# Kernel tuning notes

Measured on AMD Instinct MI355X. Metric: run time of the kernel, lower is better.

## Reference

```python
import jax, jax.numpy as jnp
import numpy as np

H = 128   # d_model / features
N = 32    # kept complex modes (d_state=64 -> 32 conjugate pairs)
B = 8
L = 8192


def setup_inputs() -> dict:
    key = jax.random.key(0)
    ks = jax.random.split(key, 8)
    x = jax.random.normal(ks[0], (B, H, L), jnp.float32)
    # S4D (diagonal SSM) kernel parameters; channels=2 for bidirectional
    C_re = (jax.random.normal(ks[1], (2, H, N), jnp.float32) * (0.5 ** 0.5))
    C_im = (jax.random.normal(ks[2], (2, H, N), jnp.float32) * (0.5 ** 0.5))
    log_A_real = jnp.log(0.5 * jnp.ones((H, N), jnp.float32))          # S4D-Lin init
    A_imag = jnp.tile(np.pi * jnp.arange(N, dtype=jnp.float32), (H, 1))
    # log_dt uniform in [log(1e-3), log(1e-1)]
    u = jax.random.uniform(ks[3], (H,), jnp.float32)
    log_dt = u * (np.log(0.1) - np.log(0.001)) + np.log(0.001)
    D = jax.random.normal(ks[4], (H,), jnp.float32)                    # skip term
    W_pw = jax.random.normal(ks[5], (H, H), jnp.float32) / np.sqrt(H)  # 1x1 conv weight (out, in)
    gamma = jnp.ones((H,), jnp.float32)
    beta = jnp.zeros((H,), jnp.float32)
    return {"x": x, "C_re": C_re, "C_im": C_im, "log_A_real": log_A_real,
            "A_imag": A_imag, "log_dt": log_dt, "D": D, "W_pw": W_pw,
            "gamma": gamma, "beta": beta}


def reference(x, C_re, C_im, log_A_real, A_imag, log_dt, D, W_pw, gamma, beta):
    Lx = x.shape[-1]
    # ---- S4D SSM kernel via Vandermonde (ZOH discretization) ----
    A = -jnp.exp(log_A_real) + 1j * A_imag                 # (H, N) complex
    dt = jnp.exp(log_dt)[:, None]                          # (H, 1)
    dtA = A * dt                                           # (H, N)
    C = C_re + 1j * C_im                                   # (2, H, N)
    Kc = C * ((jnp.exp(dtA) - 1.0) / A)                    # (2, H, N)
    vand = jnp.exp(dtA[:, :, None] * jnp.arange(Lx))       # (H, N, L)
    k = 2.0 * jnp.einsum('chn,hnl->chl', Kc, vand).real    # (2, H, L)
    # ---- bidirectional: causal half + anticausal (flipped) half ----
    k_full = (jnp.pad(k[0], ((0, 0), (0, Lx)))
              + jnp.pad(k[1][:, ::-1], ((0, 0), (Lx, 0))))  # (H, 2L)
    # ---- FFT convolution ----
    n = 2 * Lx
    y = jnp.fft.irfft(jnp.fft.rfft(x, n=n) * jnp.fft.rfft(k_full, n=n), n=n)[..., :Lx]
    y = y + x * D[:, None]                                 # skip connection
    y = jax.nn.gelu(y, approximate=False)                  # FFTConv default activation
    # ---- pointwise 1x1 conv (no bias) ----
    y = jnp.einsum('bhl,oh->bol', y, W_pw)
    # ---- BatchNorm1d (training-mode batch statistics) ----
    mean = jnp.mean(y, axis=(0, 2), keepdims=True)
    var = jnp.var(y, axis=(0, 2), keepdims=True)
    y = (y - mean) * jax.lax.rsqrt(var + 1e-5) * gamma[:, None] + beta[:, None]
    # ---- ELU + residual (dropout p=0) ----
    return jax.nn.elu(y) + x
```

## Files before the change

kernel.cpp:

```cpp
#include <hip/hip_runtime.h>
#include <math.h>

#define HCH   128
#define NMODE 32
#define BB    8
#define LLEN  8192
#define LC    256
#define CCH   (LLEN / LC)
#define ROWS  (BB * HCH)

typedef unsigned int uint;
typedef _Float16 f16x8 __attribute__((ext_vector_type(8)));
typedef float    f32x4 __attribute__((ext_vector_type(4)));

static __device__ __forceinline__ uint pk2(float a, float b) {
    union { _Float16 h[2]; uint u; } v;
    v.h[0] = (_Float16)a; v.h[1] = (_Float16)b;
    return v.u;
}

__device__ __forceinline__ float gelu_f(float y) {
    float z = fabsf(y) * 0.7071067811865476f;
    float p = fmaf(z, 0.078108f, 0.000972f);
    p = fmaf(z, p, 0.230389f);
    p = fmaf(z, p, 0.278393f);
    p = fmaf(z, p, 1.0f);
    float p2 = p * p;
    float p4 = p2 * p2;
    float er = 1.f - __builtin_amdgcn_rcpf(p4);
    float s  = copysignf(er, y);
    return 0.5f * y * (1.f + s);
}

#define DPP_ADD(v, ctrl) { int _t = __builtin_amdgcn_update_dpp(0, __float_as_int(v), \
                             (ctrl), 0xF, 0xF, true); (v) += __int_as_float(_t); }

__global__ __launch_bounds__(256) void k_prep(const float* __restrict__ C_re,
                                              const float* __restrict__ C_im,
                                              const float* __restrict__ logA,
                                              const float* __restrict__ Aim,
                                              const float* __restrict__ logdt,
                                              const float* __restrict__ W,
                                              _Float16* __restrict__ aT,
                                              _Float16* __restrict__ eT,
                                              _Float16* __restrict__ Wh,
                                              float* __restrict__ Pw,
                                              float* __restrict__ stats) {
    __shared__ float2 PL[32 * 257];
    __shared__ float4 G01[32];
    __shared__ float4 HG[32];
    __shared__ float2 WL[32];
    __shared__ float k0L[256], k1L[256];
    int tid  = threadIdx.x;
    int h    = blockIdx.x >> 1;
    int half = blockIdx.x & 1;
    if (blockIdx.x == 0) stats[tid] = 0.f;
    if (half == 0 && tid < 128) Wh[h * 128 + tid] = (_Float16)W[h * 128 + tid];
    if (tid < 32) {
        int n = tid, idx = h * 32 + n;
        float ar = expf(logA[idx]);
        float ai = Aim[idx];
        float dt = expf(logdt[h]);
        float dre = -ar * dt, dim = ai * dt;
        float er = expf(dre);
        float wr = er * cosf(dim), wi = er * sinf(dim);
        WL[n] = (float2){wr, wi};
        if (half == 0) {
            float eL = expf(dre * 256.f);
            Pw[idx]        = eL * cosf(dim * 256.f);
            Pw[4096 + idx] = eL * sinf(dim * 256.f);
        }
        float den  = ar * ar + ai * ai;
        float numr = -(wr - 1.f) * ar + wi * ai;
        float numi = -wi * ar - (wr - 1.f) * ai;
        float Kr = numr / den, Ki = numi / den;
        float c0r = C_re[idx],        c0i = C_im[idx];
        float c1r = C_re[4096 + idx], c1i = C_im[4096 + idx];
        float g0r = 2.f * (c0r * Kr - c0i * Ki), g0i = 2.f * (c0r * Ki + c0i * Kr);
        float g1r = 2.f * (c1r * Kr - c1i * Ki);
        float g1i = 2.f * (c1r * Ki + c1i * Kr);
        G01[n] = (float4){g0r, g0i, g1r, g1i};
        HG[n]  = (float4){g0r * wr - g0i * wi, g0r * wi + g0i * wr, g1r, g1i};
    }
    __syncthreads();
    {
        int n = tid & 31, tg = tid >> 5;
        float2 w = WL[n];
        float w2r = w.x * w.x - w.y * w.y,   w2i = 2.f * w.x * w.y;
        float w4r = w2r * w2r - w2i * w2i,   w4i = 2.f * w2r * w2i;
        float w8r = w4r * w4r - w4i * w4i,   w8i = 2.f * w4r * w4i;
        float pr = (tg & 1) ? w.x : 1.f;
        float pi = (tg & 1) ? w.y : 0.f;
        if (tg & 2) { float t2 = pr * w2r - pi * w2i; pi = pr * w2i + pi * w2r; pr = t2; }
        if (tg & 4) { float t4 = pr * w4r - pi * w4i; pi = pr * w4i + pi * w4r; pr = t4; }
        float2* row = &PL[n * 257];
        #pragma unroll
        for (int j = 0; j < 32; j++) {
            row[tg + 8 * j] = (float2){pr, pi};
            float tr = pr * w8r - pi * w8i; pi = pr * w8i + pi * w8r; pr = tr;
        }
    }
    __syncthreads();
    {
        int tau = tid;
        float s0 = 0.f, s1 = 0.f;
        #pragma unroll
        for (int n = 0; n < 32; n++) {
            float2 p = PL[n * 257 + tau];
            float4 g = G01[n];
            s0 += g.x * p.x - g.y * p.y;
            s1 += g.z * p.x - g.w * p.y;
        }
        k0L[tau] = s0; k1L[tau] = s1;
    }
    __syncthreads();
    #pragma unroll 4
    for (int i = 0; i < 64; i++) {
        int idx = i * 256 + tid;
        int t  = half * 128 + (idx >> 7);
        int sp = (idx & 127) << 1;
        float v0 = (sp     <= t) ? k0L[t - sp]     : k1L[sp - t - 1];
        float v1 = (sp + 1 <= t) ? k0L[t - sp - 1] : k1L[sp - t];
        *(uint*)&aT[((size_t)(h * 256 + t)) * 384 + sp] = pk2(v0, v1);
    }
    #pragma unroll 4
    for (int i = 0; i < 16; i++) {
        int idx = i * 256 + tid;
        int n = idx & 31;
        int t = half * 128 + (idx >> 5);
        float2 pt = PL[n * 257 + t];
        float2 pu = PL[n * 257 + 255 - t];
        float4 hg = HG[n];
        size_t rb = ((size_t)(h * 256 + t)) * 384;
        *(uint*)&aT[rb + 256 + 2 * n] = pk2(hg.x * pt.x - hg.y * pt.y,
                                            -(hg.x * pt.y + hg.y * pt.x));
        *(uint*)&aT[rb + 320 + 2 * n] = pk2(hg.z * pu.x - hg.w * pu.y,
                                            -(hg.z * pu.y + hg.w * pu.x));
    }
    #pragma unroll 4
    for (int i = 0; i < 16; i++) {
        int idx = i * 256 + tid;
        int n = idx >> 7;
        int s = half * 128 + (idx & 127);
        float2 ps = PL[n * 257 + s];
        float2 pu = PL[n * 257 + 255 - s];
        size_t base = (size_t)h * 128 * 256;
        eT[base + (size_t)(2 * n) * 256 + s]      = (_Float16)pu.x;
        eT[base + (size_t)(2 * n + 1) * 256 + s]  = (_Float16)pu.y;
        eT[base + (size_t)(64 + 2 * n) * 256 + s] = (_Float16)ps.x;
        eT[base + (size_t)(65 + 2 * n) * 256 + s] = (_Float16)ps.y;
    }
}

__global__ __launch_bounds__(256, 2) void k_states_c(const float* __restrict__ x,
                                                     const _Float16* __restrict__ eT,
                                                     const float* __restrict__ Pw,
                                                     _Float16* __restrict__ xh,
                                                     _Float16* __restrict__ carr) {
    __shared__ _Float16 SM[4][5120];
    int tid = threadIdx.x;
    int xcd = blockIdx.x & 7, slot = blockIdx.x >> 3;
    int h = xcd * 16 + (slot >> 1), mt = slot & 1;
    int wave = tid >> 6, lane = tid & 63;
    int wm = wave >> 1, wn = wave & 1;
    int lrow = lane & 15, quad = lane >> 4;
    int koff = quad * 8;
    f32x4 acc[4][4];
    #pragma unroll
    for (int a = 0; a < 4; a++)
        #pragma unroll
        for (int b = 0; b < 4; b++) acc[a][b] = (f32x4){0.f, 0.f, 0.f, 0.f};

    const int chA = tid >> 3, segA = tid & 7;
    const size_t xbase = (((size_t)(mt * 4) * HCH + h) << 13) + (chA << 8) + segA * 4;
    const int rB = tid >> 2, sgB = tid & 3;

    float4 ar[4]; uint4 br[2];
    #define LOADA_S(kk) { _Pragma("unroll") for (int i = 0; i < 4; i++) \
        ar[i] = *(const float4*)(x + xbase + ((size_t)i << 20) + (kk)); }
    #define LOADB_S(kk) { _Pragma("unroll") for (int i = 0; i < 2; i++) \
        br[i] = *(const uint4*)(eT + ((size_t)(h * 128 + rB + 64 * i)) * 256 + (kk) + sgB * 8); }
    #define WRITE_S(buf, kk) { _Pragma("unroll") for (int i = 0; i < 4; i++) { \
            uint2 o; o.x = pk2(ar[i].x, ar[i].y); o.y = pk2(ar[i].z, ar[i].w); \
            *(uint2*)&SM[buf][(chA + 32 * i) * 40 + segA * 4] = o; \
            *(uint2*)&xh[xbase + ((size_t)i << 20) + (kk)] = o; } \
        _Pragma("unroll") for (int i = 0; i < 2; i++) \
            *(uint4*)&SM[2 + (buf)][(rB + 64 * i) * 40 + sgB * 8] = br[i]; }

    LOADA_S(0); LOADB_S(0);
    WRITE_S(0, 0);
    __syncthreads();
    for (int kt = 0; kt < 8; kt++) {
        int cur = kt & 1;
        if (kt < 7) { LOADA_S((kt + 1) * 32); LOADB_S((kt + 1) * 32); }
        f16x8 a[4], b[4];
        #pragma unroll
        for (int f = 0; f < 4; f++) {
            a[f] = *(const f16x8*)&SM[cur][(wm * 64 + f * 16 + lrow) * 40 + koff];
            b[f] = *(const f16x8*)&SM[2 + cur][(wn * 64 + f * 16 + lrow) * 40 + koff];
        }
        #pragma unroll
        for (int fi = 0; fi < 4; fi++)
            #pragma unroll
            for (int fj = 0; fj < 4; fj++)
                acc[fi][fj] = __builtin_amdgcn_mfma_f32_16x16x32_f16(a[fi], b[fj], acc[fi][fj], 0, 0, 0);
        if (kt < 7) {
            WRITE_S(cur ^ 1, (kt + 1) * 32);
            __syncthreads();
        }
    }
    __syncthreads();
    float* Sf = (float*)SM;
    #pragma unroll
    for (int p = 0; p < 2; p++) {
        if (wm == p) {
            #pragma unroll
            for (int fi = 0; fi < 4; fi++) {
                #pragma unroll
                for (int fj = 0; fj < 4; fj++) {
                    int srow = wn * 64 + fj * 16 + lrow;
                    #pragma unroll
                    for (int rg = 0; rg < 4; rg++) {
                        int lb = fi * 16 + quad * 4 + rg;
                        Sf[lb * 128 + srow] = acc[fi][fj][rg];
                    }
                }
            }
        }
        __syncthreads();
        if (tid < 128) {
            int blocL = tid >> 6, d = (tid >> 5) & 1, n = tid & 31;
            int bloc = p * 2 + blocL;
            float wLr = Pw[h * 32 + n], wLi = Pw[4096 + h * 32 + n];
            int srow = d * 64 + 2 * n;
            float cr = 0.f, ci = 0.f;
            size_t gb = ((size_t)(h * 256 + mt * 128 + bloc * 32)) * 128 + srow;
            if (d == 0) {
                for (int c = 0; c < CCH; c++) {
                    *(uint*)&carr[gb + (size_t)c * 128] = pk2(cr, ci);
                    float2 s = *(const float2*)&Sf[(blocL * 32 + c) * 128 + srow];
                    float nr = fmaf(wLr, cr, -wLi * ci) + s.x;
                    float ni = fmaf(wLi, cr,  wLr * ci) + s.y;
                    cr = nr; ci = ni;
                }
            } else {
                for (int c = CCH - 1; c >= 0; c--) {
                    *(uint*)&carr[gb + (size_t)c * 128] = pk2(cr, ci);
                    float2 s = *(const float2*)&Sf[(blocL * 32 + c) * 128 + srow];
                    float nr = fmaf(wLr, cr, -wLi * ci) + s.x;
                    float ni = fmaf(wLi, cr,  wLr * ci) + s.y;
                    cr = nr; ci = ni;
                }
            }
        }
        __syncthreads();
    }
    #undef LOADA_S
    #undef LOADB_S
    #undef WRITE_S
}

__global__ __launch_bounds__(256, 2) void k_conv_g(const _Float16* __restrict__ xh,
                                                   const _Float16* __restrict__ aT,
                                                   const _Float16* __restrict__ carr,
                                                   const float* __restrict__ D,
                                                   _Float16* __restrict__ Yg) {
    __shared__ _Float16 At[2][128 * 40];
    __shared__ _Float16 Bt[2][128 * 40];
    int tid = threadIdx.x;
    int xcd = blockIdx.x & 7, slot = blockIdx.x >> 3;
    int p = xcd * 32 + (slot >> 1);
    int mt = slot & 1;
    int h = p >> 1, nt = p & 1;
    int wave = tid >> 6, lane = tid & 63;
    int wm = wave >> 1, wn = wave & 1;
    int lrow = lane & 15, quad = lane >> 4;
    int koff = quad * 8;
    f32x4 acc[4][4];
    #pragma unroll
    for (int a = 0; a < 4; a++)
        #pragma unroll
        for (int b = 0; b < 4; b++) acc[a][b] = (f32x4){0.f, 0.f, 0.f, 0.f};

    const int rS = tid >> 2, sgS = tid & 3;

    uint4 a_r[2], b_r[2];
    #define LOADA_C(kk) { _Pragma("unroll") for (int i = 0; i < 2; i++) { \
            int bc = mt * 128 + rS + 64 * i; \
            a_r[i] = ((kk) < 256) \
              ? *(const uint4*)(xh + (((size_t)((bc >> 5) * HCH + h)) << 13) + ((bc & 31) << 8) + (kk) + sgS * 8) \
              : *(const uint4*)(carr + ((size_t)(h * 256 + bc)) * 128 + ((kk) - 256) + sgS * 8); } }
    #define LOADB_C(kk) { _Pragma("unroll") for (int i = 0; i < 2; i++) \
        b_r[i] = *(const uint4*)(aT + ((size_t)(h * 256 + nt * 128 + rS + 64 * i)) * 384 + (kk) + sgS * 8); }
    #define WRITE_C(buf) { _Pragma("unroll") for (int i = 0; i < 2; i++) { \
            *(uint4*)&At[buf][(rS + 64 * i) * 40 + sgS * 8] = a_r[i]; \
            *(uint4*)&Bt[buf][(rS + 64 * i) * 40 + sgS * 8] = b_r[i]; } }

    LOADA_C(0); LOADB_C(0);
    WRITE_C(0);
    __syncthreads();
    for (int kt = 0; kt < 12; kt++) {
        int cur = kt & 1;
        if (kt < 11) { LOADA_C((kt + 1) * 32); LOADB_C((kt + 1) * 32); }
        f16x8 a[4], b[4];
        #pragma unroll
        for (int f = 0; f < 4; f++) {
            a[f] = *(const f16x8*)&At[cur][(wm * 64 + f * 16 + lrow) * 40 + koff];
            b[f] = *(const f16x8*)&Bt[cur][(wn * 64 + f * 16 + lrow) * 40 + koff];
        }
        #pragma unroll
        for (int fi = 0; fi < 4; fi++)
            #pragma unroll
            for (int fj = 0; fj < 4; fj++)
                acc[fi][fj] = __builtin_amdgcn_mfma_f32_16x16x32_f16(a[fi], b[fj], acc[fi][fj], 0, 0, 0);
        if (kt < 11) {
            WRITE_C(cur ^ 1);
            __syncthreads();
        }
    }
    float Dh = D[h];
    #pragma unroll
    for (int fi = 0; fi < 4; fi++) {
        #pragma unroll
        for (int fj = 0; fj < 4; fj++) {
            int t = nt * 128 + wn * 64 + fj * 16 + lrow;
            #pragma unroll
            for (int rg = 0; rg < 4; rg++) {
                int bc = mt * 128 + wm * 64 + fi * 16 + quad * 4 + rg;
                size_t base = (((size_t)((bc >> 5) * HCH + h)) << 13) + ((bc & 31) << 8) + t;
                float xv = (float)xh[base];
                float yv = acc[fi][fj][rg] + Dh * xv;
                Yg[base] = (_Float16)gelu_f(yv);
            }
        }
    }
    #undef LOADA_C
    #undef LOADB_C
    #undef WRITE_C
}

__global__ __launch_bounds__(256, 2) void k_pointwise(const _Float16* __restrict__ Yg,
                                                      const _Float16* __restrict__ Wh,
                                                      _Float16* __restrict__ z,
                                                      float* __restrict__ stats) {
    __shared__ _Float16 Yt[2][128 * 40];
    __shared__ float Ls[512];
    int tid = threadIdx.x;
    int b  = blockIdx.x >> 6;
    int l0 = (blockIdx.x & 63) << 7;
    int wave = tid >> 6, lane = tid & 63;
    int wm = wave >> 1, wn = wave & 1;
    int lrow = lane & 15, quad = lane >> 4;
    int koff = quad * 8;
    f32x4 acc[4][4];
    #pragma unroll
    for (int a = 0; a < 4; a++)
        #pragma unroll
        for (int c = 0; c < 4; c++) acc[a][c] = (f32x4){0.f, 0.f, 0.f, 0.f};

    f16x8 a[4][4];
    #pragma unroll
    for (int ks = 0; ks < 4; ks++)
        #pragma unroll
        for (int f = 0; f < 4; f++)
            a[ks][f] = *(const f16x8*)(Wh + (wm * 64 + f * 16 + lrow) * HCH + ks * 32 + koff);

    const int hhS = tid & 31;
    const int lgbase = tid >> 5;
    uint4 yv[2];
    #define LOADY(kk) { _Pragma("unroll") for (int i = 0; i < 2; i++) \
        yv[i] = *(const uint4*)(Yg + (((size_t)(b * HCH + (kk) + hhS)) << 13) + l0 + (lgbase + 8 * i) * 8); }
    #define WRITEY(buf) { _Pragma("unroll") for (int i = 0; i < 2; i++) { \
            const _Float16* hv = (const _Float16*)&yv[i]; \
            _Pragma("unroll") for (int j = 0; j < 8; j++) \
                Yt[buf][((lgbase + 8 * i) * 8 + j) * 40 + hhS] = hv[j]; } }

    LOADY(0);
    WRITEY(0);
    __syncthreads();
    for (int kt = 0; kt < 4; kt++) {
        int cur = kt & 1;
        if (kt < 3) LOADY((kt + 1) * 32);
        f16x8 bf[4];
        #pragma unroll
        for (int f = 0; f < 4; f++)
            bf[f] = *(const f16x8*)&Yt[cur][(wn * 64 + f * 16 + lrow) * 40 + koff];
        #pragma unroll
        for (int fi = 0; fi < 4; fi++)
            #pragma unroll
            for (int fj = 0; fj < 4; fj++)
                acc[fi][fj] = __builtin_amdgcn_mfma_f32_16x16x32_f16(a[kt][fi], bf[fj], acc[fi][fj], 0, 0, 0);
        if (kt < 3) {
            WRITEY(cur ^ 1);
            __syncthreads();
        }
    }
    #pragma unroll
    for (int fi = 0; fi < 4; fi++) {
        #pragma unroll
        for (int fj = 0; fj < 4; fj++) {
            int l = l0 + wn * 64 + fj * 16 + lrow;
            #pragma unroll
            for (int rg = 0; rg < 4; rg++) {
                int o = wm * 64 + fi * 16 + quad * 4 + rg;
                z[(((size_t)(b * HCH + o)) << 13) + l] = (_Float16)acc[fi][fj][rg];
            }
        }
    }
    #pragma unroll
    for (int fi = 0; fi < 4; fi++) {
        #pragma unroll
        for (int rg = 0; rg < 4; rg++) {
            float s = 0.f, q = 0.f;
            #pragma unroll
            for (int fj = 0; fj < 4; fj++) {
                float v = acc[fi][fj][rg];
                s += v; q = fmaf(v, v, q);
            }
            DPP_ADD(s, 0xB1); DPP_ADD(s, 0x4E); DPP_ADD(s, 0x141); DPP_ADD(s, 0x140);
            DPP_ADD(q, 0xB1); DPP_ADD(q, 0x4E); DPP_ADD(q, 0x141); DPP_ADD(q, 0x140);
            if (lrow == 0) {
                int olo = fi * 16 + quad * 4 + rg;
                Ls[wave * 64 + olo]       = s;
                Ls[256 + wave * 64 + olo] = q;
            }
        }
    }
    __syncthreads();
    if (tid < HCH) {
        int wmn = tid >> 6;
        int olo = tid & 63;
        float s = Ls[(wmn * 2) * 64 + olo] + Ls[(wmn * 2 + 1) * 64 + olo];
        float q = Ls[256 + (wmn * 2) * 64 + olo] + Ls[256 + (wmn * 2 + 1) * 64 + olo];
        atomicAdd(&stats[tid], s);
        atomicAdd(&stats[HCH + tid], q);
    }
    #undef LOADY
    #undef WRITEY
}

__global__ __launch_bounds__(256) void k_final(const _Float16* __restrict__ z,
                                               const float* __restrict__ x,
                                               const float* __restrict__ stats,
                                               const float* __restrict__ gamma,
                                               const float* __restrict__ beta,
                                               float* __restrict__ out) {
    size_t i8 = (size_t)blockIdx.x * 256 + threadIdx.x;
    int o = (int)((i8 >> 10) & (HCH - 1));
    const float inv_cnt = 1.f / (float)(BB * LLEN);
    float m   = stats[o] * inv_cnt;
    float var = stats[HCH + o] * inv_cnt - m * m;
    float rs  = rsqrtf(var + 1e-5f);
    float ga  = gamma[o] * rs;
    float bt  = beta[o] - m * ga;
    uint4 zv = ((const uint4*)z)[i8];
    const _Float16* zh = (const _Float16*)&zv;
    float4 xa = ((const float4*)x)[2 * i8];
    float4 xb = ((const float4*)x)[2 * i8 + 1];
    float4 ra, rb;
    { float t = fmaf((float)zh[0], ga, bt); float e = t > 0.f ? t : (__expf(t) - 1.f); ra.x = e + xa.x; }
    { float t = fmaf((float)zh[1], ga, bt); float e = t > 0.f ? t : (__expf(t) - 1.f); ra.y = e + xa.y; }
    { float t = fmaf((float)zh[2], ga, bt); float e = t > 0.f ? t : (__expf(t) - 1.f); ra.z = e + xa.z; }
    { float t = fmaf((float)zh[3], ga, bt); float e = t > 0.f ? t : (__expf(t) - 1.f); ra.w = e + xa.w; }
    { float t = fmaf((float)zh[4], ga, bt); float e = t > 0.f ? t : (__expf(t) - 1.f); rb.x = e + xb.x; }
    { float t = fmaf((float)zh[5], ga, bt); float e = t > 0.f ? t : (__expf(t) - 1.f); rb.y = e + xb.y; }
    { float t = fmaf((float)zh[6], ga, bt); float e = t > 0.f ? t : (__expf(t) - 1.f); rb.z = e + xb.z; }
    { float t = fmaf((float)zh[7], ga, bt); float e = t > 0.f ? t : (__expf(t) - 1.f); rb.w = e + xb.w; }
    ((float4*)out)[2 * i8]     = ra;
    ((float4*)out)[2 * i8 + 1] = rb;
}

extern "C" void kernel_launch(void* const* d_in, const int* in_sizes, int n_in,
                              void* d_out, int out_size, void* d_ws, size_t ws_size,
                              hipStream_t stream) {
    const float* x     = (const float*)d_in[0];
    const float* C_re  = (const float*)d_in[1];
    const float* C_im  = (const float*)d_in[2];
    const float* logA  = (const float*)d_in[3];
    const float* Aim   = (const float*)d_in[4];
    const float* logdt = (const float*)d_in[5];
    const float* D     = (const float*)d_in[6];
    const float* W     = (const float*)d_in[7];
    const float* gamma = (const float*)d_in[8];
    const float* beta  = (const float*)d_in[9];

    float* ws = (float*)d_ws;
    _Float16* eT    = (_Float16*)ws;
    _Float16* Yg    = (_Float16*)ws;
    _Float16* aT    = (_Float16*)(ws + 8388608);
    _Float16* zf    = (_Float16*)(ws + 8388608);
    _Float16* carr  = (_Float16*)(ws + 16777216);
    float*    Pw    = ws + 16777216 + 2097152;
    float*    stats = Pw + 8192;
    _Float16* Wh    = (_Float16*)(ws + 18882880);
    _Float16* xh    = (_Float16*)(ws + 18891072);
    float*    out   = (float*)d_out;

    k_prep     <<<256,  256, 0, stream>>>(C_re, C_im, logA, Aim, logdt, W, aT, eT, Wh, Pw, stats);
    k_states_c <<<256,  256, 0, stream>>>(x, eT, Pw, xh, carr);
    k_conv_g   <<<512,  256, 0, stream>>>(xh, aT, carr, D, Yg);
    k_pointwise<<<512,  256, 0, stream>>>(Yg, Wh, zf, stats);
    k_final    <<<4096, 256, 0, stream>>>(zf, x, stats, gamma, beta, out);
}
```

Before: 175.5 us.

## Replace materialized Toeplitz kernel matrix with LDS-built Toeplitz fragments; split states kernel

The 256x256 Toeplitz block of the SSM kernel is no longer written to global memory per channel. Instead a compact 512-element packed kernel vector is stored, and the conv kernel builds the B fragments directly from LDS using shifted indices with even and odd packed copies. This removes large global write and read traffic for the Toeplitz operand. The states kernel is also split across two blocks per (h, mt), one per direction, doubling the grid and removing the serialized two-phase scan. The cost is extra LDS loads in the conv inner loop and duplicated x loads in the states kernel.

```diff
diff --git a/kernel.cpp b/kernel.cpp
--- a/kernel.cpp
+++ b/kernel.cpp
@@ -41,7 +41,8 @@
                                               const float* __restrict__ Aim,
                                               const float* __restrict__ logdt,
                                               const float* __restrict__ W,
-                                              _Float16* __restrict__ aT,
+                                              _Float16* __restrict__ cT,
+                                              uint* __restrict__ kmg,
                                               _Float16* __restrict__ eT,
                                               _Float16* __restrict__ Wh,
                                               float* __restrict__ Pw,
@@ -51,6 +52,7 @@
     __shared__ float4 HG[32];
     __shared__ float2 WL[32];
     __shared__ float k0L[256], k1L[256];
+    __shared__ _Float16 KMl[516];
     int tid  = threadIdx.x;
     int h    = blockIdx.x >> 1;
     int half = blockIdx.x & 1;
@@ -114,14 +116,18 @@
         k0L[tau] = s0; k1L[tau] = s1;
     }
     __syncthreads();
-    #pragma unroll 4
-    for (int i = 0; i < 64; i++) {
-        int idx = i * 256 + tid;
-        int t  = half * 128 + (idx >> 7);
-        int sp = (idx & 127) << 1;
-        float v0 = (sp     <= t) ? k0L[t - sp]     : k1L[sp - t - 1];
-        float v1 = (sp + 1 <= t) ? k0L[t - sp - 1] : k1L[sp - t];
-        *(uint*)&aT[((size_t)(h * 256 + t)) * 384 + sp] = pk2(v0, v1);
+    if (half == 0) {
+        KMl[tid]       = (_Float16)k0L[255 - tid];
+        KMl[256 + tid] = (_Float16)k1L[tid];
+        if (tid == 0) { KMl[512] = (_Float16)0.f; KMl[513] = (_Float16)0.f; }
+    }
+    __syncthreads();
+    if (half == 0) {
+        union { _Float16 hh[2]; uint u; } pa, pb;
+        pa.hh[0] = KMl[2 * tid];     pa.hh[1] = KMl[2 * tid + 1];
+        pb.hh[0] = KMl[2 * tid + 1]; pb.hh[1] = KMl[2 * tid + 2];
+        kmg[(size_t)h * 512 + tid]       = pa.u;
+        kmg[(size_t)h * 512 + 256 + tid] = pb.u;
     }
     #pragma unroll 4
     for (int i = 0; i < 16; i++) {
@@ -131,11 +137,11 @@
         float2 pt = PL[n * 257 + t];
         float2 pu = PL[n * 257 + 255 - t];
         float4 hg = HG[n];
-        size_t rb = ((size_t)(h * 256 + t)) * 384;
-        *(uint*)&aT[rb + 256 + 2 * n] = pk2(hg.x * pt.x - hg.y * pt.y,
-                                            -(hg.x * pt.y + hg.y * pt.x));
-        *(uint*)&aT[rb + 320 + 2 * n] = pk2(hg.z * pu.x - hg.w * pu.y,
-                                            -(hg.z * pu.y + hg.w * pu.x));
+        size_t rb = ((size_t)(h * 256 + t)) * 128;
+        *(uint*)&cT[rb + 2 * n]      = pk2(hg.x * pt.x - hg.y * pt.y,
+                                           -(hg.x * pt.y + hg.y * pt.x));
+        *(uint*)&cT[rb + 64 + 2 * n] = pk2(hg.z * pu.x - hg.w * pu.y,
+                                           -(hg.z * pu.y + hg.w * pu.x));
     }
     #pragma unroll 4
     for (int i = 0; i < 16; i++) {
@@ -157,35 +163,35 @@
                                                      const float* __restrict__ Pw,
                                                      _Float16* __restrict__ xh,
                                                      _Float16* __restrict__ carr) {
-    __shared__ _Float16 SM[4][5120];
+    __shared__ float Sf[128 * 66];
+    _Float16* SMh = (_Float16*)Sf;
     int tid = threadIdx.x;
     int xcd = blockIdx.x & 7, slot = blockIdx.x >> 3;
-    int h = xcd * 16 + (slot >> 1), mt = slot & 1;
+    int h = xcd * 16 + (slot >> 2);
+    int mt = (slot >> 1) & 1, d = slot & 1;
     int wave = tid >> 6, lane = tid & 63;
     int wm = wave >> 1, wn = wave & 1;
     int lrow = lane & 15, quad = lane >> 4;
     int koff = quad * 8;
-    f32x4 acc[4][4];
+    f32x4 acc[4][2];
     #pragma unroll
     for (int a = 0; a < 4; a++)
         #pragma unroll
-        for (int b = 0; b < 4; b++) acc[a][b] = (f32x4){0.f, 0.f, 0.f, 0.f};
+        for (int b = 0; b < 2; b++) acc[a][b] = (f32x4){0.f, 0.f, 0.f, 0.f};
 
     const int chA = tid >> 3, segA = tid & 7;
     const size_t xbase = (((size_t)(mt * 4) * HCH + h) << 13) + (chA << 8) + segA * 4;
     const int rB = tid >> 2, sgB = tid & 3;
 
-    float4 ar[4]; uint4 br[2];
+    float4 ar[4]; uint4 br;
     #define LOADA_S(kk) { _Pragma("unroll") for (int i = 0; i < 4; i++) \
         ar[i] = *(const float4*)(x + xbase + ((size_t)i << 20) + (kk)); }
-    #define LOADB_S(kk) { _Pragma("unroll") for (int i = 0; i < 2; i++) \
-        br[i] = *(const uint4*)(eT + ((size_t)(h * 128 + rB + 64 * i)) * 256 + (kk) + sgB * 8); }
+    #define LOADB_S(kk) { br = *(const uint4*)(eT + ((size_t)(h * 128 + d * 64 + rB)) * 256 + (kk) + sgB * 8); }
     #define WRITE_S(buf, kk) { _Pragma("unroll") for (int i = 0; i < 4; i++) { \
             uint2 o; o.x = pk2(ar[i].x, ar[i].y); o.y = pk2(ar[i].z, ar[i].w); \
-            *(uint2*)&SM[buf][(chA + 32 * i) * 40 + segA * 4] = o; \
-            *(uint2*)&xh[xbase + ((size_t)i << 20) + (kk)] = o; } \
-        _Pragma("unroll") for (int i = 0; i < 2; i++) \
-            *(uint4*)&SM[2 + (buf)][(rB + 64 * i) * 40 + sgB * 8] = br[i]; }
+            *(uint2*)&SMh[(buf) * 5120 + (chA + 32 * i) * 40 + segA * 4] = o; \
+            if (d == 0) *(uint2*)&xh[xbase + ((size_t)i << 20) + (kk)] = o; } \
+        *(uint4*)&SMh[10240 + (buf) * 2560 + rB * 40 + sgB * 8] = br; }
 
     LOADA_S(0); LOADB_S(0);
     WRITE_S(0, 0);
@@ -193,16 +199,17 @@
     for (int kt = 0; kt < 8; kt++) {
         int cur = kt & 1;
         if (kt < 7) { LOADA_S((kt + 1) * 32); LOADB_S((kt + 1) * 32); }
-        f16x8 a[4], b[4];
-        #pragma unroll
-        for (int f = 0; f < 4; f++) {
-            a[f] = *(const f16x8*)&SM[cur][(wm * 64 + f * 16 + lrow) * 40 + koff];
-            b[f] = *(const f16x8*)&SM[2 + cur][(wn * 64 + f * 16 + lrow) * 40 + koff];
-        }
+        f16x8 a[4], b[2];
+        #pragma unroll
+        for (int f = 0; f < 4; f++)
+            a[f] = *(const f16x8*)&SMh[cur * 5120 + (wm * 64 + f * 16 + lrow) * 40 + koff];
+        #pragma unroll
+        for (int f = 0; f < 2; f++)
+            b[f] = *(const f16x8*)&SMh[10240 + cur * 2560 + (wn * 32 + f * 16 + lrow) * 40 + koff];
         #pragma unroll
         for (int fi = 0; fi < 4; fi++)
             #pragma unroll
-            for (int fj = 0; fj < 4; fj++)
+            for (int fj = 0; fj < 2; fj++)
                 acc[fi][fj] = __builtin_amdgcn_mfma_f32_16x16x32_f16(a[fi], b[fj], acc[fi][fj], 0, 0, 0);
         if (kt < 7) {
             WRITE_S(cur ^ 1, (kt + 1) * 32);
@@ -210,50 +217,41 @@
         }
     }
     __syncthreads();
-    float* Sf = (float*)SM;
-    #pragma unroll
-    for (int p = 0; p < 2; p++) {
-        if (wm == p) {
-            #pragma unroll
-            for (int fi = 0; fi < 4; fi++) {
-                #pragma unroll
-                for (int fj = 0; fj < 4; fj++) {
-                    int srow = wn * 64 + fj * 16 + lrow;
-                    #pragma unroll
-                    for (int rg = 0; rg < 4; rg++) {
-                        int lb = fi * 16 + quad * 4 + rg;
-                        Sf[lb * 128 + srow] = acc[fi][fj][rg];
-                    }
-                }
-            }
-        }
-        __syncthreads();
-        if (tid < 128) {
-            int blocL = tid >> 6, d = (tid >> 5) & 1, n = tid & 31;
-            int bloc = p * 2 + blocL;
-            float wLr = Pw[h * 32 + n], wLi = Pw[4096 + h * 32 + n];
-            int srow = d * 64 + 2 * n;
-            float cr = 0.f, ci = 0.f;
-            size_t gb = ((size_t)(h * 256 + mt * 128 + bloc * 32)) * 128 + srow;
-            if (d == 0) {
-                for (int c = 0; c < CCH; c++) {
-                    *(uint*)&carr[gb + (size_t)c * 128] = pk2(cr, ci);
-                    float2 s = *(const float2*)&Sf[(blocL * 32 + c) * 128 + srow];
-                    float nr = fmaf(wLr, cr, -wLi * ci) + s.x;
-                    float ni = fmaf(wLi, cr,  wLr * ci) + s.y;
-                    cr = nr; ci = ni;
-                }
-            } else {
-                for (int c = CCH - 1; c >= 0; c--) {
-                    *(uint*)&carr[gb + (size_t)c * 128] = pk2(cr, ci);
-                    float2 s = *(const float2*)&Sf[(blocL * 32 + c) * 128 + srow];
-                    float nr = fmaf(wLr, cr, -wLi * ci) + s.x;
-                    float ni = fmaf(wLi, cr,  wLr * ci) + s.y;
-                    cr = nr; ci = ni;
-                }
-            }
-        }
-        __syncthreads();
+    #pragma unroll
+    for (int fi = 0; fi < 4; fi++) {
+        #pragma unroll
+        for (int fj = 0; fj < 2; fj++) {
+            int srow = wn * 32 + fj * 16 + lrow;
+            #pragma unroll
+            for (int rg = 0; rg < 4; rg++) {
+                int bc = wm * 64 + fi * 16 + quad * 4 + rg;
+                Sf[bc * 66 + srow] = acc[fi][fj][rg];
+            }
+        }
+    }
+    __syncthreads();
+    if (tid < 128) {
+        int bloc = tid >> 5, n = tid & 31;
+        float wLr = Pw[h * 32 + n], wLi = Pw[4096 + h * 32 + n];
+        float cr = 0.f, ci = 0.f;
+        size_t gb = ((size_t)(h * 256 + mt * 128 + bloc * 32)) * 128 + d * 64 + 2 * n;
+        if (d == 0) {
+            for (int c = 0; c < CCH; c++) {
+                *(uint*)&carr[gb + (size_t)c * 128] = pk2(cr, ci);
+                float2 s = *(const float2*)&Sf[(bloc * 32 + c) * 66 + 2 * n];
+                float nr = fmaf(wLr, cr, -wLi * ci) + s.x;
+                float ni = fmaf(wLi, cr,  wLr * ci) + s.y;
+                cr = nr; ci = ni;
+            }
+        } else {
+            for (int c = CCH - 1; c >= 0; c--) {
+                *(uint*)&carr[gb + (size_t)c * 128] = pk2(cr, ci);
+                float2 s = *(const float2*)&Sf[(bloc * 32 + c) * 66 + 2 * n];
+                float nr = fmaf(wLr, cr, -wLi * ci) + s.x;
+                float ni = fmaf(wLi, cr,  wLr * ci) + s.y;
+                cr = nr; ci = ni;
+            }
+        }
     }
     #undef LOADA_S
     #undef LOADB_S
@@ -261,12 +259,14 @@
 }
 
 __global__ __launch_bounds__(256, 2) void k_conv_g(const _Float16* __restrict__ xh,
-                                                   const _Float16* __restrict__ aT,
+                                                   const uint* __restrict__ kmg,
+                                                   const _Float16* __restrict__ cT,
                                                    const _Float16* __restrict__ carr,
                                                    const float* __restrict__ D,
                                                    _Float16* __restrict__ Yg) {
     __shared__ _Float16 At[2][128 * 40];
     __shared__ _Float16 Bt[2][128 * 40];
+    __shared__ uint KMA[256], KMB[256];
     int tid = threadIdx.x;
     int xcd = blockIdx.x & 7, slot = blockIdx.x >> 3;
     int p = xcd * 32 + (slot >> 1);
@@ -291,22 +291,44 @@
               ? *(const uint4*)(xh + (((size_t)((bc >> 5) * HCH + h)) << 13) + ((bc & 31) << 8) + (kk) + sgS * 8) \
               : *(const uint4*)(carr + ((size_t)(h * 256 + bc)) * 128 + ((kk) - 256) + sgS * 8); } }
     #define LOADB_C(kk) { _Pragma("unroll") for (int i = 0; i < 2; i++) \
-        b_r[i] = *(const uint4*)(aT + ((size_t)(h * 256 + nt * 128 + rS + 64 * i)) * 384 + (kk) + sgS * 8); }
-    #define WRITE_C(buf) { _Pragma("unroll") for (int i = 0; i < 2; i++) { \
-            *(uint4*)&At[buf][(rS + 64 * i) * 40 + sgS * 8] = a_r[i]; \
-            *(uint4*)&Bt[buf][(rS + 64 * i) * 40 + sgS * 8] = b_r[i]; } }
-
-    LOADA_C(0); LOADB_C(0);
-    WRITE_C(0);
+        b_r[i] = *(const uint4*)(cT + ((size_t)(h * 256 + nt * 128 + rS + 64 * i)) * 128 + ((kk) - 256) + sgS * 8); }
+    #define WRITE_A(buf) { _Pragma("unroll") for (int i = 0; i < 2; i++) \
+        *(uint4*)&At[buf][(rS + 64 * i) * 40 + sgS * 8] = a_r[i]; }
+    #define WRITE_B(buf) { _Pragma("unroll") for (int i = 0; i < 2; i++) \
+        *(uint4*)&Bt[buf][(rS + 64 * i) * 40 + sgS * 8] = b_r[i]; }
+
+    KMA[tid] = kmg[(size_t)h * 512 + tid];
+    KMB[tid] = kmg[(size_t)h * 512 + 256 + tid];
+    LOADA_C(0);
+    WRITE_A(0);
     __syncthreads();
     for (int kt = 0; kt < 12; kt++) {
         int cur = kt & 1;
-        if (kt < 11) { LOADA_C((kt + 1) * 32); LOADB_C((kt + 1) * 32); }
+        if (kt < 11) {
+            LOADA_C((kt + 1) * 32);
+            if (kt + 1 >= 8) LOADB_C((kt + 1) * 32);
+        }
         f16x8 a[4], b[4];
         #pragma unroll
-        for (int f = 0; f < 4; f++) {
+        for (int f = 0; f < 4; f++)
             a[f] = *(const f16x8*)&At[cur][(wm * 64 + f * 16 + lrow) * 40 + koff];
-            b[f] = *(const f16x8*)&Bt[cur][(wn * 64 + f * 16 + lrow) * 40 + koff];
+        if (kt < 8) {
+            int kk = kt * 32;
+            #pragma unroll
+            for (int f = 0; f < 4; f++) {
+                int t_f = nt * 128 + wn * 64 + f * 16 + lrow;
+                int idx0 = 255 - t_f + kk + koff;
+                int par = idx0 & 1;
+                int dw = idx0 >> 1;
+                const uint* kp = par ? KMB : KMA;
+                union { uint u[4]; f16x8 v; } bu;
+                bu.u[0] = kp[dw]; bu.u[1] = kp[dw + 1]; bu.u[2] = kp[dw + 2]; bu.u[3] = kp[dw + 3];
+                b[f] = bu.v;
+            }
+        } else {
+            #pragma unroll
+            for (int f = 0; f < 4; f++)
+                b[f] = *(const f16x8*)&Bt[cur][(wn * 64 + f * 16 + lrow) * 40 + koff];
         }
         #pragma unroll
         for (int fi = 0; fi < 4; fi++)
@@ -314,7 +336,8 @@
             for (int fj = 0; fj < 4; fj++)
                 acc[fi][fj] = __builtin_amdgcn_mfma_f32_16x16x32_f16(a[fi], b[fj], acc[fi][fj], 0, 0, 0);
         if (kt < 11) {
-            WRITE_C(cur ^ 1);
+            WRITE_A(cur ^ 1);
+            if (kt + 1 >= 8) WRITE_B(cur ^ 1);
             __syncthreads();
         }
     }
@@ -336,7 +359,8 @@
     }
     #undef LOADA_C
     #undef LOADB_C
-    #undef WRITE_C
+    #undef WRITE_A
+    #undef WRITE_B
 }
 
 __global__ __launch_bounds__(256, 2) void k_pointwise(const _Float16* __restrict__ Yg,
@@ -487,8 +511,9 @@
     float* ws = (float*)d_ws;
     _Float16* eT    = (_Float16*)ws;
     _Float16* Yg    = (_Float16*)ws;
-    _Float16* aT    = (_Float16*)(ws + 8388608);
     _Float16* zf    = (_Float16*)(ws + 8388608);
+    _Float16* cT    = (_Float16*)(ws + 12582912);
+    uint*     kmg   = (uint*)(ws + 14680064);
     _Float16* carr  = (_Float16*)(ws + 16777216);
     float*    Pw    = ws + 16777216 + 2097152;
     float*    stats = Pw + 8192;
@@ -496,9 +521,9 @@
     _Float16* xh    = (_Float16*)(ws + 18891072);
     float*    out   = (float*)d_out;
 
-    k_prep     <<<256,  256, 0, stream>>>(C_re, C_im, logA, Aim, logdt, W, aT, eT, Wh, Pw, stats);
-    k_states_c <<<256,  256, 0, stream>>>(x, eT, Pw, xh, carr);
-    k_conv_g   <<<512,  256, 0, stream>>>(xh, aT, carr, D, Yg);
+    k_prep     <<<256,  256, 0, stream>>>(C_re, C_im, logA, Aim, logdt, W, cT, kmg, eT, Wh, Pw, stats);
+    k_states_c <<<512,  256, 0, stream>>>(x, eT, Pw, xh, carr);
+    k_conv_g   <<<512,  256, 0, stream>>>(xh, kmg, cT, carr, D, Yg);
     k_pointwise<<<512,  256, 0, stream>>>(Yg, Wh, zf, stats);
     k_final    <<<4096, 256, 0, stream>>>(zf, x, stats, gamma, beta, out);
 }
```

New measurement: 178.4 us. About the same (+1.6%).
